# Kernel optimization log

Measured on AMD Instinct MI355X. Metric: run time of the kernel, lower is better.

## Reference

```python
import jax, jax.numpy as jnp
import numpy as np

B, N, NPOINT, NSAMPLE = 8, 8192, 2048, 32
RADIUS = 0.4
C_IN = 64
MLP = [64, 64, 128]
EPS = 1e-5
BIG = 1e10


def setup_inputs() -> dict:
    key = jax.random.key(0)
    ks = jax.random.split(key, 2 + 4 * len(MLP))
    inp = {
        'xyz': jax.random.normal(ks[0], (B, N, 3), jnp.float32),
        'features': jax.random.normal(ks[1], (B, C_IN, N), jnp.float32),
    }
    last_c = C_IN + 3
    j = 2
    for i, out_c in enumerate(MLP):
        inp[f'w{i}'] = jax.random.normal(ks[j], (out_c, last_c), jnp.float32) * (1.0 / np.sqrt(last_c)); j += 1
        inp[f'b{i}'] = jax.random.normal(ks[j], (out_c,), jnp.float32) * 0.01; j += 1
        inp[f'g{i}'] = 1.0 + 0.01 * jax.random.normal(ks[j], (out_c,), jnp.float32); j += 1
        inp[f'bt{i}'] = 0.01 * jax.random.normal(ks[j], (out_c,), jnp.float32); j += 1
        last_c = out_c
    return inp


def fps(xyz, m):
    # Farthest point sampling; deterministic start at index 0 (torch uses randint).
    b, n, _ = xyz.shape

    def step(carry, _):
        dist, far = carry
        centroid = jnp.take_along_axis(xyz, far[:, None, None], axis=1)  # [B,1,3]
        d = jnp.sum((xyz - centroid) ** 2, axis=-1)                      # [B,N]
        dist = jnp.minimum(dist, d)
        new_far = jnp.argmax(dist, axis=1)
        return (dist, new_far), far

    init = (jnp.full((b, n), BIG, xyz.dtype), jnp.zeros((b,), jnp.int32))
    _, idxs = jax.lax.scan(step, init, None, length=m)
    return jnp.transpose(idxs)  # [B,m]


def ball_query(xyz, centroids, radius, k):
    # Euclidean cdist via the (a-b)^2 = a^2 + b^2 - 2ab expansion.
    x2 = jnp.sum(xyz * xyz, axis=-1)            # [B,N]
    c2 = jnp.sum(centroids * centroids, axis=-1)  # [B,M]
    d2 = c2[:, :, None] + x2[:, None, :] - 2.0 * jnp.einsum('bmd,bnd->bmn', centroids, xyz)
    d = jnp.sqrt(jnp.maximum(d2, 0.0))           # [B,M,N]
    dm = jnp.where(d <= radius, d, BIG)
    _, idx = jax.lax.top_k(-dm, k)               # k smallest distances
    return idx                                   # [B,M,K]


def gather_points(x, idx):
    # x: [B,N,C], idx: [B,M,K] -> [B,M,K,C]
    b = x.shape[0]
    return x[jnp.arange(b)[:, None, None], idx]


def reference(xyz, features, w0, b0, g0, bt0, w1, b1, g1, bt1, w2, b2, g2, bt2):
    idx = fps(xyz, NPOINT)                                   # [B,M]
    new_xyz = jnp.take_along_axis(xyz, idx[:, :, None], axis=1)  # [B,M,3]
    knn_idx = ball_query(xyz, new_xyz, RADIUS, NSAMPLE)      # [B,M,K]
    grouped_xyz = gather_points(xyz, knn_idx)                # [B,M,K,3]
    grouped_xyz_norm = grouped_xyz - new_xyz[:, :, None, :]
    grouped_feat = gather_points(jnp.transpose(features, (0, 2, 1)), knn_idx)  # [B,M,K,C]
    feat = jnp.concatenate([grouped_xyz_norm, grouped_feat], axis=-1)          # [B,M,K,C+3]

    for w, b, g, bt in ((w0, b0, g0, bt0), (w1, b1, g1, bt1), (w2, b2, g2, bt2)):
        feat = jnp.einsum('bmkc,oc->bmko', feat, w) + b      # 1x1 conv
        mu = jnp.mean(feat, axis=(0, 1, 2))                  # BN, training-mode batch stats
        var = jnp.mean((feat - mu) ** 2, axis=(0, 1, 2))
        feat = (feat - mu) * jax.lax.rsqrt(var + EPS) * g + bt
        feat = jax.nn.relu(feat)

    new_feat = jnp.max(feat, axis=2)                         # max over neighbors -> [B,M,C_out]
    return new_xyz, jnp.transpose(new_feat, (0, 2, 1))       # [B,M,3], [B,C_out,M]
```

## Files before the change

kernel.cpp:

```cpp
#include <hip/hip_runtime.h>
#include <hip/hip_bf16.h>
#include <stdint.h>

typedef unsigned short u16;
typedef unsigned int   u32;
typedef unsigned long long u64;
typedef float v2f __attribute__((ext_vector_type(2)));
typedef __attribute__((ext_vector_type(8))) short bf16x8;
typedef __attribute__((ext_vector_type(4))) float f32x4;

#define B_    8
#define N_    8192
#define M_    2048
#define NS_   32
#define CIN_  64
#define ROWS_ (B_*M_*NS_)
#define BIGF  1e10f
#define EPSF  1e-5f
#define INV_ROWS (1.0f/524288.0f)

__device__ __forceinline__ u16 f2bf(float f){
  u32 x=__float_as_uint(f);
  return (u16)((x + 0x7FFFu + ((x>>16)&1u))>>16);
}
__device__ __forceinline__ float bf2f(u16 u){ return __uint_as_float(((u32)u)<<16); }

__device__ __forceinline__ u64 wave_max_key(u64 k){
#define DPP_LVL(CTRL) { \
    u32 lo_=(u32)__builtin_amdgcn_update_dpp(0,(int)(u32)k,(CTRL),0xF,0xF,true); \
    u32 hi_=(u32)__builtin_amdgcn_update_dpp(0,(int)(u32)(k>>32),(CTRL),0xF,0xF,true); \
    u64 o_=((u64)hi_<<32)|(u64)lo_; \
    k=(o_>k)?o_:k; }
  DPP_LVL(0x111)
  DPP_LVL(0x112)
  DPP_LVL(0x114)
  DPP_LVL(0x118)
  DPP_LVL(0x142)
  DPP_LVL(0x143)
#undef DPP_LVL
  return k;
}

__global__ __launch_bounds__(256) void k_prep(
    const float* w0,const float* b0,const float* g0,const float* bt0,
    const float* w1,const float* b1,const float* g1,const float* bt1,
    const float* w2,const float* b2,const float* g2,const float* bt2,
    float* Wt0,float* Wt1,float* Wt2,
    float* biasf,float* gf,float* btf,float* stats,
    u16* Wb1h, u16* Wb1l, u16* Wb2h, u16* Wb2l)
{
  int tid=threadIdx.x;
  for (int i=tid;i<768;i+=256) stats[i]=0.f;
  for (int i=tid;i<67*64;i+=256){ int c=i>>6,o=i&63;  Wt0[c*64+o]=w0[o*67+c]; }
  for (int i=tid;i<64*64;i+=256){ int c=i>>6,o=i&63;  Wt1[c*64+o]=w1[o*64+c]; }
  for (int i=tid;i<64*128;i+=256){int c=i>>7,o=i&127; Wt2[c*128+o]=w2[o*64+c]; }
  for (int i=tid;i<4096;i+=256){
    int e=i&7, lane=(i>>3)&63, k0=(i>>9)&1, tn=i>>10;
    int col = tn*16 + (lane&15);
    int k   = k0*32 + ((lane>>4)&3)*8 + e;
    float v = w1[col*64 + k];
    u16 hib = f2bf(v);
    Wb1h[i] = hib;
    Wb1l[i] = f2bf(v - bf2f(hib));
  }
  for (int i=tid;i<8192;i+=256){
    int e=i&7, lane=(i>>3)&63, k0=(i>>9)&1, tn=i>>10;
    int col = tn*16 + (lane&15);
    int k   = k0*32 + ((lane>>4)&3)*8 + e;
    float v = w2[col*64 + k];
    u16 hib = f2bf(v);
    Wb2h[i] = hib;
    Wb2l[i] = f2bf(v - bf2f(hib));
  }
  if (tid<64){
    biasf[0*128+tid]=b0[tid]; gf[0*128+tid]=g0[tid]; btf[0*128+tid]=bt0[tid];
    biasf[1*128+tid]=b1[tid]; gf[1*128+tid]=g1[tid]; btf[1*128+tid]=bt1[tid];
  }
  if (tid<128){
    biasf[2*128+tid]=b2[tid]; gf[2*128+tid]=g2[tid]; btf[2*128+tid]=bt2[tid];
  }
}

__global__ __launch_bounds__(256) void k_tr(const float* __restrict__ feats, u16* __restrict__ featT)
{
  __shared__ float t[64][65];
  int bb=blockIdx.y, n0=blockIdx.x*64, tid=threadIdx.x;
  int a=tid&63, q=tid>>6;
  const float* fp = feats + (size_t)bb*CIN_*N_;
  #pragma unroll
  for (int s=0;s<16;s++){ int c=q*16+s; t[c][a]=fp[(size_t)c*N_ + n0 + a]; }
  __syncthreads();
  u16* op = featT + (size_t)bb*N_*CIN_;
  #pragma unroll
  for (int s=0;s<16;s++){ int n=q*16+s; op[(size_t)(n0+n)*CIN_ + a] = f2bf(t[a][n]); }
}

__global__ __launch_bounds__(512) void k_fps(const float* __restrict__ xyz,
                                             float* __restrict__ nxyz, float* __restrict__ out0)
{
#pragma clang fp contract(off)
  __shared__ float sx[N_], sy[N_], sz[N_];
  __shared__ int sidx[M_];
  __shared__ u64 skey[2][8];
  int b=blockIdx.x, tid=threadIdx.x;
  const float* xp = xyz + (size_t)b*N_*3;
  for (int i=tid;i<N_;i+=512){ sx[i]=xp[i*3]; sy[i]=xp[i*3+1]; sz[i]=xp[i*3+2]; }
  __syncthreads();
  v2f px[8],py[8],pz[8],md[8];
  int base = tid*16;
  #pragma unroll
  for (int p=0;p<8;p++){
    px[p]=*(const v2f*)&sx[base+2*p];
    py[p]=*(const v2f*)&sy[base+2*p];
    pz[p]=*(const v2f*)&sz[base+2*p];
    v2f m0; m0[0]=BIGF; m0[1]=BIGF; md[p]=m0;
  }
  u32 invb = 0xFFFFFFFFu - (u32)base;
  int far=0;
  int lane=tid&63, wv=tid>>6;
  for (int step=0; step<M_; step++){
    if (tid==0) sidx[step]=far;
    float cxs=sx[far], cys=sy[far], czs=sz[far];
    v2f cx; cx[0]=cxs; cx[1]=cxs;
    v2f cy; cy[0]=cys; cy[1]=cys;
    v2f cz; cz[0]=czs; cz[1]=czs;
    u64 kb=0;
    #pragma unroll
    for (int p=0;p<8;p++){
      v2f dx=px[p]-cx, dy=py[p]-cy, dz=pz[p]-cz;
      v2f d=(dx*dx+dy*dy)+dz*dz;
      v2f m=__builtin_elementwise_min(md[p],d);
      md[p]=m;
      u64 k0=((u64)__float_as_uint(m[0])<<32)|(u64)(invb-(u32)(2*p));
      u64 k1=((u64)__float_as_uint(m[1])<<32)|(u64)(invb-(u32)(2*p+1));
      u64 kp=(k1>k0)?k1:k0;
      kb=(kp>kb)?kp:kb;
    }
    kb = wave_max_key(kb);
    int par = step & 1;
    if (lane==63) skey[par][wv]=kb;
    __syncthreads();
    u64 a0=skey[par][0],a1=skey[par][1],a2=skey[par][2],a3=skey[par][3];
    u64 a4=skey[par][4],a5=skey[par][5],a6=skey[par][6],a7=skey[par][7];
    a0=(a1>a0)?a1:a0; a2=(a3>a2)?a3:a2; a4=(a5>a4)?a5:a4; a6=(a7>a6)?a7:a6;
    a0=(a2>a0)?a2:a0; a4=(a6>a4)?a6:a4;
    a0=(a4>a0)?a4:a0;
    far = (int)(0xFFFFFFFFu - (u32)(a0 & 0xFFFFFFFFull));
  }
  for (int i=tid;i<M_;i+=512){
    int id = sidx[i];
    float x=sx[id], y=sy[id], z=sz[id];
    size_t o=(size_t)(b*M_+i)*3;
    nxyz[o]=x; nxyz[o+1]=y; nxyz[o+2]=z;
    out0[o]=x; out0[o+1]=y; out0[o+2]=z;
  }
}

#define BQCAP 512
__global__ __launch_bounds__(512) void k_bq(const float* __restrict__ xyz, const float* __restrict__ nxyz,
                                            int* __restrict__ knn)
{
  __shared__ float4 sP[N_];
  __shared__ float candd[8][BQCAP];
  __shared__ u16  candi[8][BQCAP];
  int tid=threadIdx.x;
  int cid0 = blockIdx.x*8;
  int b = cid0 >> 11;
  const float* xp = xyz + (size_t)b*N_*3;
  for (int i=tid;i<N_;i+=512){
    float x=xp[i*3], y=xp[i*3+1], z=xp[i*3+2];
    float x2 = __fmul_rn(x,x);
    x2 = __fadd_rn(x2, __fmul_rn(y,y));
    x2 = __fadd_rn(x2, __fmul_rn(z,z));
    sP[i]=make_float4(x,y,z,x2);
  }
  __syncthreads();
  int w=tid>>6, lane=tid&63;
  int cid = cid0 + w;
  float cx=nxyz[(size_t)cid*3], cy=nxyz[(size_t)cid*3+1], cz=nxyz[(size_t)cid*3+2];
  float c2 = __fmul_rn(cx,cx);
  c2 = __fadd_rn(c2, __fmul_rn(cy,cy));
  c2 = __fadd_rn(c2, __fmul_rn(cz,cz));
  int cnt=0;
  for (int i0=0;i0<N_;i0+=64){
    int i=i0+lane;
    float4 p=sP[i];
    float dot = __fmul_rn(cx,p.x);
    dot = __fadd_rn(dot, __fmul_rn(cy,p.y));
    dot = __fadd_rn(dot, __fmul_rn(cz,p.z));
    float d2 = __fsub_rn(__fadd_rn(c2,p.w), __fmul_rn(2.0f,dot));
    float d = sqrtf(fmaxf(d2,0.f));
    bool in = (d <= 0.4f);
    u64 msk = __ballot(in);
    int pos = cnt + __popcll(msk & ((1ull<<lane)-1ull));
    if (in && pos<BQCAP){ candd[w][pos]=d; candi[w][pos]=(u16)i; }
    cnt += __popcll(msk);
  }
  int R = cnt<BQCAP ? cnt : BQCAP;
  int* kout = knn + (size_t)cid*NS_;
  if (R >= NS_){
    for (int s=0;s<NS_;s++){
      u64 kb = ~0ull;
      for (int j=lane;j<R;j+=64){
        float v=candd[w][j];
        u64 k = ((u64)__float_as_uint(v)<<32) | (u64)(u32)j;
        kb = (k<kb)?k:kb;
      }
      u64 inv = wave_max_key(~kb);
      if (lane==63){
        u64 kw = ~inv;
        int bpp = (int)(u32)(kw & 0xFFFFFFFFull);
        kout[s]=candi[w][bpp];
        candd[w][bpp]=3e38f;
      }
    }
  } else {
    if (lane<R) kout[lane]=candi[w][lane];
    int need = NS_-R, slot = R;
    for (int i0=0; i0<N_ && need>0; i0+=64){
      int i=i0+lane;
      float4 p=sP[i];
      float dot = __fmul_rn(cx,p.x);
      dot = __fadd_rn(dot, __fmul_rn(cy,p.y));
      dot = __fadd_rn(dot, __fmul_rn(cz,p.z));
      float d2 = __fsub_rn(__fadd_rn(c2,p.w), __fmul_rn(2.0f,dot));
      float d = sqrtf(fmaxf(d2,0.f));
      bool in = (d <= 0.4f);
      u64 mm = __ballot(!in);
      while (mm && need>0){
        int bpos = __ffsll((long long)mm)-1;
        if (lane==0) kout[slot] = i0+bpos;
        slot++; need--;
        mm &= mm-1;
      }
    }
  }
}

__global__ __launch_bounds__(256) void k_mm0(const float* __restrict__ xyz, const u16* __restrict__ featT,
                                             const int* __restrict__ knn, const float* __restrict__ nxyz,
                                             const float* __restrict__ Wt0, const float* __restrict__ biasf,
                                             u16* __restrict__ Y0)
{
  __shared__ u16 Xs[256*70];
  __shared__ float Wl[67*64];
  int tid=threadIdx.x;
  for (int i=tid;i<67*64;i+=256) Wl[i]=Wt0[i];
  int base = blockIdx.x*256;
  {
    int row = base + tid;
    int bm  = row >> 5;
    int b   = row >> 16;
    int n   = knn[row];
    const float* cp = nxyz + (size_t)bm*3;
    const float* xp = xyz + ((size_t)b*N_ + n)*3;
    u16* xr = &Xs[tid*70];
    xr[0]=f2bf(xp[0]-cp[0]);
    xr[1]=f2bf(xp[1]-cp[1]);
    xr[2]=f2bf(xp[2]-cp[2]);
    const uint4* fp = (const uint4*)(featT + ((size_t)b*N_ + n)*CIN_);
    #pragma unroll
    for (int i=0;i<8;i++){
      uint4 v=fp[i];
      u16* d = xr + 3 + i*8;
      d[0]=(u16)(v.x&0xFFFFu); d[1]=(u16)(v.x>>16);
      d[2]=(u16)(v.y&0xFFFFu); d[3]=(u16)(v.y>>16);
      d[4]=(u16)(v.z&0xFFFFu); d[5]=(u16)(v.z>>16);
      d[6]=(u16)(v.w&0xFFFFu); d[7]=(u16)(v.w>>16);
    }
  }
  __syncthreads();
  int g=tid>>7, rt=tid&127;
  float acc0[32], acc1[32];
  #pragma unroll
  for (int j=0;j<32;j++){ acc0[j]=0.f; acc1[j]=0.f; }
  const u16* xa=&Xs[rt*70];
  const u16* xb=&Xs[(rt+128)*70];
  for (int c=0;c<67;c++){
    float a=bf2f(xa[c]);
    float bx=bf2f(xb[c]);
    const float4* wr=(const float4*)&Wl[c*64 + g*32];
    #pragma unroll
    for (int o=0;o<8;o++){
      float4 wv=wr[o];
      acc0[o*4+0]+=a*wv.x;  acc0[o*4+1]+=a*wv.y;  acc0[o*4+2]+=a*wv.z;  acc0[o*4+3]+=a*wv.w;
      acc1[o*4+0]+=bx*wv.x; acc1[o*4+1]+=bx*wv.y; acc1[o*4+2]+=bx*wv.z; acc1[o*4+3]+=bx*wv.w;
    }
  }
  float bb[32];
  #pragma unroll
  for (int j=0;j<32;j++) bb[j]=biasf[g*32+j];
  u16* y0p = Y0 + ((size_t)(base+rt))*64 + g*32;
  u16* y1p = Y0 + ((size_t)(base+rt+128))*64 + g*32;
  #pragma unroll
  for (int j=0;j<32;j++){
    y0p[j]=f2bf(acc0[j]+bb[j]);
    y1p[j]=f2bf(acc1[j]+bb[j]);
  }
}

template<int C>
__global__ __launch_bounds__(256) void k_stats(const u16* __restrict__ Y, float* __restrict__ statsOut)
{
  __shared__ float sred[4][128];
  int tid=threadIdx.x;
  int c0=(tid&7)*8;
  int rg=tid>>3;
  float s[8], ss[8];
  #pragma unroll
  for (int k=0;k<8;k++){ s[k]=0.f; ss[k]=0.f; }
  for (size_t r=(size_t)blockIdx.x*32+rg; r<ROWS_; r+=(size_t)gridDim.x*32){
    uint4 v=*(const uint4*)&Y[r*64+c0];
    u32 a[4]={v.x,v.y,v.z,v.w};
    #pragma unroll
    for (int q=0;q<4;q++){
      float lo=bf2f((u16)(a[q]&0xFFFFu));
      float hi=bf2f((u16)(a[q]>>16));
      s[q*2]+=lo;   ss[q*2]+=lo*lo;
      s[q*2+1]+=hi; ss[q*2+1]+=hi*hi;
    }
  }
  #pragma unroll
  for (int off=32; off>=8; off>>=1){
    #pragma unroll
    for (int k=0;k<8;k++){
      s[k]+=__shfl_down(s[k],off);
      ss[k]+=__shfl_down(ss[k],off);
    }
  }
  int lane=tid&63, wv=tid>>6;
  if (lane<8){
    #pragma unroll
    for (int k=0;k<8;k++){
      int ch=lane*8+k;
      sred[wv][ch]=s[k];
      sred[wv][64+ch]=ss[k];
    }
  }
  __syncthreads();
  if (tid<128){
    float a=sred[0][tid]+sred[1][tid]+sred[2][tid]+sred[3][tid];
    int ch=tid&63, which=tid>>6;
    atomicAdd(&statsOut[ch*2+which], a);
  }
}

__global__ __launch_bounds__(256) void k_mm1(u16* __restrict__ Y,
                                             const u16* __restrict__ Wb1h, const u16* __restrict__ Wb1l,
                                             const float* __restrict__ bias1, const float* __restrict__ gf0,
                                             const float* __restrict__ btf0, const float* __restrict__ stats0)
{
  __shared__ u16 Xs[64*64];
  __shared__ u16 WH[8*64*8];
  __shared__ u16 WL[8*64*8];
  __shared__ float sc[64], sh[64];
  int tid=threadIdx.x;
  if (tid<64){
    float mu = stats0[tid*2]*INV_ROWS;
    float var= stats0[tid*2+1]*INV_ROWS - mu*mu;
    float rs = 1.0f/sqrtf(var+EPSF);
    float s  = rs*gf0[tid];
    sc[tid]=s; sh[tid]=btf0[tid]-mu*s;
  }
  {
    const uint4* sh4=(const uint4*)Wb1h; uint4* dh4=(uint4*)WH;
    const uint4* sl4=(const uint4*)Wb1l; uint4* dl4=(uint4*)WL;
    dh4[tid]=sh4[tid]; dh4[tid+256]=sh4[tid+256];
    dl4[tid]=sl4[tid]; dl4[tid+256]=sl4[tid+256];
  }
  __syncthreads();
  size_t base=(size_t)blockIdx.x*64;
  for (int i=tid;i<512;i+=256){
    int rl=i>>3, c0=(i&7)*8;
    uint4 v=*(const uint4*)(Y + (base+rl)*64 + c0);
    u32 arr[4]={v.x,v.y,v.z,v.w};
    u32 pk[4];
    #pragma unroll
    for (int q=0;q<4;q++){
      int cc=c0+q*2;
      float lo=bf2f((u16)(arr[q]&0xFFFFu));
      float hi=bf2f((u16)(arr[q]>>16));
      lo=fmaxf(0.f, lo*sc[cc]+sh[cc]);
      hi=fmaxf(0.f, hi*sc[cc+1]+sh[cc+1]);
      pk[q] = (u32)f2bf(lo) | ((u32)f2bf(hi)<<16);
    }
    uint4 o4; o4.x=pk[0]; o4.y=pk[1]; o4.z=pk[2]; o4.w=pk[3];
    int byteoff = rl*128 + ((c0*2) ^ ((rl&7)<<4));
    *(uint4*)((char*)Xs + byteoff) = o4;
  }
  __syncthreads();
  int w=tid>>6, lane=tid&63;
  f32x4 acc[4];
  #pragma unroll
  for (int tn=0;tn<4;tn++){ acc[tn][0]=0.f; acc[tn][1]=0.f; acc[tn][2]=0.f; acc[tn][3]=0.f; }
  int arow = w*16 + (lane&15);
  #pragma unroll
  for (int k0=0;k0<2;k0++){
    int aoff = arow*128 + ((k0*64 + (lane>>4)*16) ^ ((arow&7)<<4));
    bf16x8 a = *(const bf16x8*)((const char*)Xs + aoff);
    #pragma unroll
    for (int tn=0;tn<4;tn++){
      bf16x8 bl = *(const bf16x8*)&WL[((tn*2+k0)*64+lane)*8];
      bf16x8 bh = *(const bf16x8*)&WH[((tn*2+k0)*64+lane)*8];
      acc[tn] = __builtin_amdgcn_mfma_f32_16x16x32_bf16(a, bl, acc[tn], 0,0,0);
      acc[tn] = __builtin_amdgcn_mfma_f32_16x16x32_bf16(a, bh, acc[tn], 0,0,0);
    }
  }
  #pragma unroll
  for (int tn=0;tn<4;tn++){
    int col = tn*16 + (lane&15);
    float bb = bias1[col];
    #pragma unroll
    for (int j=0;j<4;j++){
      int row = w*16 + (lane>>4)*4 + j;
      Y[(base+row)*64 + col] = f2bf(acc[tn][j] + bb);
    }
  }
}

__global__ __launch_bounds__(256) void k_mm2a(const u16* __restrict__ Y1,
                                              const u16* __restrict__ Wb2h, const u16* __restrict__ Wb2l,
                                              const float* __restrict__ bias2, const float* __restrict__ gf1,
                                              const float* __restrict__ btf1, const float* __restrict__ stats1,
                                              float* __restrict__ stats2, float* __restrict__ out1)
{
  __shared__ u16 Xs[64*64];
  __shared__ u16 WH[8192];
  __shared__ u16 WL[8192];
  __shared__ float Ys[64*128];
  __shared__ float sc[64], sh[64];
  __shared__ float sred[512];
  int tid=threadIdx.x;
  if (tid<64){
    float mu = stats1[tid*2]*INV_ROWS;
    float var= stats1[tid*2+1]*INV_ROWS - mu*mu;
    float rs = 1.0f/sqrtf(var+EPSF);
    float s  = rs*gf1[tid];
    sc[tid]=s; sh[tid]=btf1[tid]-mu*s;
  }
  {
    const uint4* s4=(const uint4*)Wb2h; uint4* d4=(uint4*)WH;
    const uint4* s5=(const uint4*)Wb2l; uint4* d5=(uint4*)WL;
    for (int i=tid;i<1024;i+=256){ d4[i]=s4[i]; d5[i]=s5[i]; }
  }
  int w=tid>>6, lane=tid&63;
  int pg=tid>>7, po=tid&127;
  float bias_po_unused; (void)bias_po_unused;
  float accSum=0.f, accSq=0.f;
  __syncthreads();
  for (int tile=blockIdx.x; tile<8192; tile+=gridDim.x){
    size_t base=(size_t)tile*64;
    for (int i=tid;i<512;i+=256){
      int rl=i>>3, c0=(i&7)*8;
      uint4 v=*(const uint4*)(Y1 + (base+rl)*64 + c0);
      u32 arr[4]={v.x,v.y,v.z,v.w};
      u32 pk[4];
      #pragma unroll
      for (int q=0;q<4;q++){
        int cc=c0+q*2;
        float lo=bf2f((u16)(arr[q]&0xFFFFu));
        float hi=bf2f((u16)(arr[q]>>16));
        lo=fmaxf(0.f, lo*sc[cc]+sh[cc]);
        hi=fmaxf(0.f, hi*sc[cc+1]+sh[cc+1]);
        pk[q] = (u32)f2bf(lo) | ((u32)f2bf(hi)<<16);
      }
      uint4 o4; o4.x=pk[0]; o4.y=pk[1]; o4.z=pk[2]; o4.w=pk[3];
      int byteoff = rl*128 + ((c0*2) ^ ((rl&7)<<4));
      *(uint4*)((char*)Xs + byteoff) = o4;
    }
    __syncthreads();
    f32x4 acc[8];
    #pragma unroll
    for (int tn=0;tn<8;tn++){ acc[tn][0]=0.f; acc[tn][1]=0.f; acc[tn][2]=0.f; acc[tn][3]=0.f; }
    int arow = w*16 + (lane&15);
    #pragma unroll
    for (int k0=0;k0<2;k0++){
      int aoff = arow*128 + ((k0*64 + (lane>>4)*16) ^ ((arow&7)<<4));
      bf16x8 a = *(const bf16x8*)((const char*)Xs + aoff);
      #pragma unroll
      for (int tn=0;tn<8;tn++){
        bf16x8 bl = *(const bf16x8*)&WL[((tn*2+k0)*64+lane)*8];
        bf16x8 bh = *(const bf16x8*)&WH[((tn*2+k0)*64+lane)*8];
        acc[tn] = __builtin_amdgcn_mfma_f32_16x16x32_bf16(a, bl, acc[tn], 0,0,0);
        acc[tn] = __builtin_amdgcn_mfma_f32_16x16x32_bf16(a, bh, acc[tn], 0,0,0);
      }
    }
    #pragma unroll
    for (int tn=0;tn<8;tn++){
      int col = tn*16 + (lane&15);
      float bb = bias2[col];
      #pragma unroll
      for (int j=0;j<4;j++){
        int row = w*16 + (lane>>4)*4 + j;
        int byteoff = row*512 + ((col*4) ^ ((row&7)<<4));
        *(float*)((char*)Ys + byteoff) = acc[tn][j] + bb;
      }
    }
    __syncthreads();
    {
      float mx=-3e38f;
      #pragma unroll 4
      for (int k=0;k<32;k++){
        int row = pg*32 + k;
        int byteoff = row*512 + ((po*4) ^ ((row&7)<<4));
        float y = *(const float*)((const char*)Ys + byteoff);
        accSum += y; accSq += y*y;
        mx = fmaxf(mx, y);
      }
      int bm = tile*2 + pg; int bi = bm>>11, m = bm&2047;
      out1[((size_t)bi*128+po)*M_ + m] = mx;
    }
    __syncthreads();
  }
  sred[tid]      = accSum;
  sred[256+tid]  = accSq;
  __syncthreads();
  if (tid<128){
    float s = sred[tid] + sred[tid+128];
    float q = sred[256+tid] + sred[256+tid+128];
    atomicAdd(&stats2[tid*2],   s);
    atomicAdd(&stats2[tid*2+1], q);
  }
}

__global__ __launch_bounds__(256) void k_pool(float* __restrict__ out1, const float* __restrict__ stats2,
                                              const float* __restrict__ gf2, const float* __restrict__ btf2)
{
  int idx = blockIdx.x*256 + threadIdx.x;
  int o = (idx >> 11) & 127;
  float mu = stats2[o*2]*INV_ROWS;
  float var= stats2[o*2+1]*INV_ROWS - mu*mu;
  float rs = 1.0f/sqrtf(var+EPSF);
  float s  = rs*gf2[o];
  float sh = btf2[o]-mu*s;
  out1[idx] = fmaxf(0.f, out1[idx]*s + sh);
}

extern "C" void kernel_launch(void* const* d_in, const int* in_sizes, int n_in,
                              void* d_out, int out_size, void* d_ws, size_t ws_size,
                              hipStream_t stream)
{
  (void)in_sizes; (void)n_in; (void)out_size; (void)ws_size;
  const float* xyz =(const float*)d_in[0];
  const float* feat=(const float*)d_in[1];
  const float* w0=(const float*)d_in[2],  *b0=(const float*)d_in[3],  *g0=(const float*)d_in[4],  *bt0=(const float*)d_in[5];
  const float* w1=(const float*)d_in[6],  *b1=(const float*)d_in[7],  *g1=(const float*)d_in[8],  *bt1=(const float*)d_in[9];
  const float* w2=(const float*)d_in[10], *b2=(const float*)d_in[11], *g2=(const float*)d_in[12], *bt2=(const float*)d_in[13];
  float* out0=(float*)d_out;
  float* out1=out0 + (size_t)B_*M_*3;

  char* ws=(char*)d_ws;
  float* nxyz =(float*)(ws);
  u16*   Wb1h =(u16*)  (ws + 196608);
  u16*   Wb1l =(u16*)  (ws + 204800);
  u16*   Wb2h =(u16*)  (ws + 212992);
  u16*   Wb2l =(u16*)  (ws + 229376);
  int*   knn  =(int*)  (ws + 262144);
  float* Wt0  =(float*)(ws + 2359296);
  float* Wt1  =(float*)(ws + 2376704);
  float* Wt2  =(float*)(ws + 2393088);
  float* biasf=(float*)(ws + 2425856);
  float* gfp  =(float*)(ws + 2427392);
  float* btfp =(float*)(ws + 2428928);
  float* stats=(float*)(ws + 2430464);
  u16*   featT=(u16*)  (ws + 2433536);
  u16*   Y0   =(u16*)  (ws + 10822144);

  k_prep<<<1,256,0,stream>>>(w0,b0,g0,bt0,w1,b1,g1,bt1,w2,b2,g2,bt2,Wt0,Wt1,Wt2,biasf,gfp,btfp,stats,
                             Wb1h,Wb1l,Wb2h,Wb2l);
  k_tr<<<dim3(128,8),256,0,stream>>>(feat, featT);
  k_fps<<<B_,512,0,stream>>>(xyz, nxyz, out0);
  k_bq<<<2048,512,0,stream>>>(xyz, nxyz, knn);
  k_mm0<<<2048,256,0,stream>>>(xyz, featT, knn, nxyz, Wt0, biasf+0, Y0);
  k_stats<64><<<128,256,0,stream>>>(Y0, stats+0);
  k_mm1<<<8192,256,0,stream>>>(Y0, Wb1h, Wb1l, biasf+128, gfp+0, btfp+0, stats+0);
  k_stats<64><<<128,256,0,stream>>>(Y0, stats+256);
  k_mm2a<<<512,256,0,stream>>>(Y0, Wb2h, Wb2l, biasf+256, gfp+128, btfp+128, stats+256, stats+512, out1);
  k_pool<<<8192,256,0,stream>>>(out1, stats+512, gfp+256, btfp+256);
}
```

Before: 2.360 ms.

## Rewrite first MLP layer as bf16 MFMA GEMM with split-weight precision

Replaces the scalar FMA layer-0 conv with MFMA 16x16x32 bf16 instructions, using hi/lo bf16 splits of the weights prepacked in k_prep into the MFMA fragment layout. The K dimension is reordered with features first and xyz last, padded from 67 to 96. Gathered rows are staged in XOR-swizzled LDS with 64 rows per block, so the grid grows to 8192 blocks. This removes the FP32 ALU cost of the first GEMM but adds padding work and two MFMAs per tile.

```diff
diff --git a/kernel.cpp b/kernel.cpp
--- a/kernel.cpp
+++ b/kernel.cpp
@@ -45,15 +45,23 @@
     const float* w0,const float* b0,const float* g0,const float* bt0,
     const float* w1,const float* b1,const float* g1,const float* bt1,
     const float* w2,const float* b2,const float* g2,const float* bt2,
-    float* Wt0,float* Wt1,float* Wt2,
     float* biasf,float* gf,float* btf,float* stats,
-    u16* Wb1h, u16* Wb1l, u16* Wb2h, u16* Wb2l)
+    u16* Wb0h, u16* Wb0l, u16* Wb1h, u16* Wb1l, u16* Wb2h, u16* Wb2l)
 {
   int tid=threadIdx.x;
   for (int i=tid;i<768;i+=256) stats[i]=0.f;
-  for (int i=tid;i<67*64;i+=256){ int c=i>>6,o=i&63;  Wt0[c*64+o]=w0[o*67+c]; }
-  for (int i=tid;i<64*64;i+=256){ int c=i>>6,o=i&63;  Wt1[c*64+o]=w1[o*64+c]; }
-  for (int i=tid;i<64*128;i+=256){int c=i>>7,o=i&127; Wt2[c*128+o]=w2[o*64+c]; }
+  for (int i=tid;i<6144;i+=256){
+    int e=i&7, lane=(i>>3)&63, idx=i>>9;
+    int tn=idx/3, k0=idx%3;
+    int col = tn*16 + (lane&15);
+    int k   = k0*32 + ((lane>>4)&3)*8 + e;
+    float v = 0.f;
+    if (k < 64)            v = w0[col*67 + 3 + k];
+    else if (k < 67)       v = w0[col*67 + (k-64)];
+    u16 hib = f2bf(v);
+    Wb0h[i] = hib;
+    Wb0l[i] = f2bf(v - bf2f(hib));
+  }
   for (int i=tid;i<4096;i+=256){
     int e=i&7, lane=(i>>3)&63, k0=(i>>9)&1, tn=i>>10;
     int col = tn*16 + (lane&15);
@@ -239,63 +247,68 @@
 
 __global__ __launch_bounds__(256) void k_mm0(const float* __restrict__ xyz, const u16* __restrict__ featT,
                                              const int* __restrict__ knn, const float* __restrict__ nxyz,
-                                             const float* __restrict__ Wt0, const float* __restrict__ biasf,
-                                             u16* __restrict__ Y0)
-{
-  __shared__ u16 Xs[256*70];
-  __shared__ float Wl[67*64];
+                                             const u16* __restrict__ Wb0h, const u16* __restrict__ Wb0l,
+                                             const float* __restrict__ bias0, u16* __restrict__ Y0)
+{
+  __shared__ u16 Xs[64*128];
+  __shared__ u16 WH[12*64*8];
+  __shared__ u16 WL[12*64*8];
   int tid=threadIdx.x;
-  for (int i=tid;i<67*64;i+=256) Wl[i]=Wt0[i];
-  int base = blockIdx.x*256;
   {
-    int row = base + tid;
-    int bm  = row >> 5;
-    int b   = row >> 16;
-    int n   = knn[row];
-    const float* cp = nxyz + (size_t)bm*3;
-    const float* xp = xyz + ((size_t)b*N_ + n)*3;
-    u16* xr = &Xs[tid*70];
-    xr[0]=f2bf(xp[0]-cp[0]);
-    xr[1]=f2bf(xp[1]-cp[1]);
-    xr[2]=f2bf(xp[2]-cp[2]);
+    const uint4* s4=(const uint4*)Wb0h; uint4* d4=(uint4*)WH;
+    const uint4* s5=(const uint4*)Wb0l; uint4* d5=(uint4*)WL;
+    for (int i=tid;i<768;i+=256){ d4[i]=s4[i]; d5[i]=s5[i]; }
+  }
+  size_t base=(size_t)blockIdx.x*64;
+  {
+    int rl=tid>>2, t=tid&3;
+    int row=(int)base+rl;
+    int bm = row>>5, b = row>>16;
+    int n  = knn[row];
     const uint4* fp = (const uint4*)(featT + ((size_t)b*N_ + n)*CIN_);
-    #pragma unroll
-    for (int i=0;i<8;i++){
-      uint4 v=fp[i];
-      u16* d = xr + 3 + i*8;
-      d[0]=(u16)(v.x&0xFFFFu); d[1]=(u16)(v.x>>16);
-      d[2]=(u16)(v.y&0xFFFFu); d[3]=(u16)(v.y>>16);
-      d[4]=(u16)(v.z&0xFFFFu); d[5]=(u16)(v.z>>16);
-      d[6]=(u16)(v.w&0xFFFFu); d[7]=(u16)(v.w>>16);
-    }
-  }
-  __syncthreads();
-  int g=tid>>7, rt=tid&127;
-  float acc0[32], acc1[32];
-  #pragma unroll
-  for (int j=0;j<32;j++){ acc0[j]=0.f; acc1[j]=0.f; }
-  const u16* xa=&Xs[rt*70];
-  const u16* xb=&Xs[(rt+128)*70];
-  for (int c=0;c<67;c++){
-    float a=bf2f(xa[c]);
-    float bx=bf2f(xb[c]);
-    const float4* wr=(const float4*)&Wl[c*64 + g*32];
-    #pragma unroll
-    for (int o=0;o<8;o++){
-      float4 wv=wr[o];
-      acc0[o*4+0]+=a*wv.x;  acc0[o*4+1]+=a*wv.y;  acc0[o*4+2]+=a*wv.z;  acc0[o*4+3]+=a*wv.w;
-      acc1[o*4+0]+=bx*wv.x; acc1[o*4+1]+=bx*wv.y; acc1[o*4+2]+=bx*wv.z; acc1[o*4+3]+=bx*wv.w;
-    }
-  }
-  float bb[32];
-  #pragma unroll
-  for (int j=0;j<32;j++) bb[j]=biasf[g*32+j];
-  u16* y0p = Y0 + ((size_t)(base+rt))*64 + g*32;
-  u16* y1p = Y0 + ((size_t)(base+rt+128))*64 + g*32;
-  #pragma unroll
-  for (int j=0;j<32;j++){
-    y0p[j]=f2bf(acc0[j]+bb[j]);
-    y1p[j]=f2bf(acc1[j]+bb[j]);
+    char* xr = (char*)Xs + rl*256;
+    u32 swz = (u32)((rl&7)<<4);
+    uint4 v0=fp[t*2], v1=fp[t*2+1];
+    *(uint4*)(xr + ((t*32)    ^ swz)) = v0;
+    *(uint4*)(xr + ((t*32+16) ^ swz)) = v1;
+    uint4 pz = make_uint4(0u,0u,0u,0u);
+    if (t==0){
+      const float* cp = nxyz + (size_t)bm*3;
+      const float* xp = xyz + ((size_t)b*N_ + n)*3;
+      u32 w01 = (u32)f2bf(xp[0]-cp[0]) | ((u32)f2bf(xp[1]-cp[1])<<16);
+      u32 w2  = (u32)f2bf(xp[2]-cp[2]);
+      pz.x = w01; pz.y = w2;
+    }
+    *(uint4*)(xr + ((128+t*16) ^ swz)) = pz;
+  }
+  __syncthreads();
+  int w=tid>>6, lane=tid&63;
+  f32x4 acc[4];
+  #pragma unroll
+  for (int tn=0;tn<4;tn++){ acc[tn][0]=0.f; acc[tn][1]=0.f; acc[tn][2]=0.f; acc[tn][3]=0.f; }
+  int arow = w*16 + (lane&15);
+  u32 aswz = (u32)((arow&7)<<4);
+  #pragma unroll
+  for (int k0=0;k0<3;k0++){
+    int aoff = arow*256 + (int)(((u32)((k0*32 + ((lane>>4)&3)*8)*2)) ^ aswz);
+    bf16x8 a = *(const bf16x8*)((const char*)Xs + aoff);
+    #pragma unroll
+    for (int tn=0;tn<4;tn++){
+      bf16x8 bl = *(const bf16x8*)&WL[((tn*3+k0)*64+lane)*8];
+      bf16x8 bh = *(const bf16x8*)&WH[((tn*3+k0)*64+lane)*8];
+      acc[tn] = __builtin_amdgcn_mfma_f32_16x16x32_bf16(a, bl, acc[tn], 0,0,0);
+      acc[tn] = __builtin_amdgcn_mfma_f32_16x16x32_bf16(a, bh, acc[tn], 0,0,0);
+    }
+  }
+  #pragma unroll
+  for (int tn=0;tn<4;tn++){
+    int col = tn*16 + (lane&15);
+    float bb = bias0[col];
+    #pragma unroll
+    for (int j=0;j<4;j++){
+      int row = w*16 + (lane>>4)*4 + j;
+      Y0[(base+row)*64 + col] = f2bf(acc[tn][j] + bb);
+    }
   }
 }
 
@@ -445,7 +458,6 @@
   }
   int w=tid>>6, lane=tid&63;
   int pg=tid>>7, po=tid&127;
-  float bias_po_unused; (void)bias_po_unused;
   float accSum=0.f, accSq=0.f;
   __syncthreads();
   for (int tile=blockIdx.x; tile<8192; tile+=gridDim.x){
@@ -556,9 +568,8 @@
   u16*   Wb2h =(u16*)  (ws + 212992);
   u16*   Wb2l =(u16*)  (ws + 229376);
   int*   knn  =(int*)  (ws + 262144);
-  float* Wt0  =(float*)(ws + 2359296);
-  float* Wt1  =(float*)(ws + 2376704);
-  float* Wt2  =(float*)(ws + 2393088);
+  u16*   Wb0h =(u16*)  (ws + 2359296);
+  u16*   Wb0l =(u16*)  (ws + 2376704);
   float* biasf=(float*)(ws + 2425856);
   float* gfp  =(float*)(ws + 2427392);
   float* btfp =(float*)(ws + 2428928);
@@ -566,12 +577,12 @@
   u16*   featT=(u16*)  (ws + 2433536);
   u16*   Y0   =(u16*)  (ws + 10822144);
 
-  k_prep<<<1,256,0,stream>>>(w0,b0,g0,bt0,w1,b1,g1,bt1,w2,b2,g2,bt2,Wt0,Wt1,Wt2,biasf,gfp,btfp,stats,
-                             Wb1h,Wb1l,Wb2h,Wb2l);
+  k_prep<<<1,256,0,stream>>>(w0,b0,g0,bt0,w1,b1,g1,bt1,w2,b2,g2,bt2,biasf,gfp,btfp,stats,
+                             Wb0h,Wb0l,Wb1h,Wb1l,Wb2h,Wb2l);
   k_tr<<<dim3(128,8),256,0,stream>>>(feat, featT);
   k_fps<<<B_,512,0,stream>>>(xyz, nxyz, out0);
   k_bq<<<2048,512,0,stream>>>(xyz, nxyz, knn);
-  k_mm0<<<2048,256,0,stream>>>(xyz, featT, knn, nxyz, Wt0, biasf+0, Y0);
+  k_mm0<<<8192,256,0,stream>>>(xyz, featT, knn, nxyz, Wb0h, Wb0l, biasf+0, Y0);
   k_stats<64><<<128,256,0,stream>>>(Y0, stats+0);
   k_mm1<<<8192,256,0,stream>>>(Y0, Wb1h, Wb1l, biasf+128, gfp+0, btfp+0, stats+0);
   k_stats<64><<<128,256,0,stream>>>(Y0, stats+256);
```

Result: no change. 2.316 ms (-1.9%).
